# Kernel tuning notes

Hardware: AMD Instinct MI355X
Metric: run time of the kernel (lower is better)

Reference implementation:

```python
import jax, jax.numpy as jnp
import numpy as np
from jax.scipy.special import erf

N = 8_388_608  # number of options in the book
R = 0.02       # risk-free rate (init arg r)
Q = 0.01       # dividend yield (init arg q)


def setup_inputs() -> dict:
    key = jax.random.key(0)
    k1, k2, k3, k4 = jax.random.split(key, 4)
    S0 = jax.random.uniform(k1, (N,), jnp.float32, 80.0, 120.0)
    K = jax.random.uniform(k2, (N,), jnp.float32, 80.0, 120.0)
    T = jax.random.uniform(k3, (N,), jnp.float32, 0.01, 2.0)
    vt = jax.random.uniform(k4, (N,), jnp.float32, 0.01, 0.2)
    return {"S0": S0, "K": K, "T": T, "vt": vt}


def reference(S0, K, T, vt):
    # Black-Scholes 'all' pricing: [n,4] = (call, put, digital_call, digital_put)
    inv_sqrt2 = 0.7071067811865476
    sv = jnp.sqrt(vt * T)
    d1 = (jnp.log(S0 / K) + (R - Q + vt * 0.5) * T) / sv
    d2 = d1 - sv
    N1 = 0.5 * (1.0 + erf(d1 * inv_sqrt2))
    N2 = 0.5 * (1.0 + erf(d2 * inv_sqrt2))
    disc_r = jnp.exp(-R * T)
    disc_q = jnp.exp(-Q * T)
    call = S0 * disc_q * N1 - K * disc_r * N2
    put = -S0 * disc_q * (1.0 - N1) + K * disc_r * (1.0 - N2)
    dig_call = disc_r * N2
    dig_put = disc_r * (1.0 - N2)
    # expired (T == 0) branch: intrinsic values / indicator payoffs
    expired = T == 0
    call = jnp.where(expired, jnp.maximum(S0 - K, 0.0), call)
    put = jnp.where(expired, jnp.maximum(K - S0, 0.0), put)
    dig_call = jnp.where(expired, (S0 > K).astype(S0.dtype), dig_call)
    dig_put = jnp.where(expired, (S0 <= K).astype(S0.dtype), dig_put)
    return jnp.stack([call, put, dig_call, dig_put], axis=-1)
```

## Files before the change

kernel.cpp:

```cpp
#include <hip/hip_runtime.h>
#include <hip/hip_bf16.h>


#define BS_R 0.02f
#define BS_Q 0.01f

__device__ __forceinline__ void bs_one(float s, float k, float t, float v,
                                       float4& o) {
    const float inv_sqrt2 = 0.7071067811865476f;
    float sv = sqrtf(v * t);
    float d1 = (logf(s / k) + (BS_R - BS_Q + v * 0.5f) * t) / sv;
    float d2 = d1 - sv;
    float N1 = 0.5f * (1.0f + erff(d1 * inv_sqrt2));
    float N2 = 0.5f * (1.0f + erff(d2 * inv_sqrt2));
    float disc_r = expf(-BS_R * t);
    float disc_q = expf(-BS_Q * t);
    float call = s * disc_q * N1 - k * disc_r * N2;
    float put  = -s * disc_q * (1.0f - N1) + k * disc_r * (1.0f - N2);
    float dc = disc_r * N2;
    float dp = disc_r * (1.0f - N2);
    bool expired = (t == 0.0f);
    if (expired) {
        call = fmaxf(s - k, 0.0f);
        put  = fmaxf(k - s, 0.0f);
        dc   = (s > k) ? 1.0f : 0.0f;
        dp   = (s <= k) ? 1.0f : 0.0f;
    }
    o.x = call; o.y = put; o.z = dc; o.w = dp;
}

__global__ void __launch_bounds__(256)
bs_all_kernel(const float4* __restrict__ S0, const float4* __restrict__ K,
              const float4* __restrict__ T, const float4* __restrict__ vt,
              float4* __restrict__ out, int n4) {
    int stride = gridDim.x * blockDim.x;
    for (int i = blockIdx.x * blockDim.x + threadIdx.x; i < n4; i += stride) {
        float4 s = S0[i];
        float4 k = K[i];
        float4 t = T[i];
        float4 v = vt[i];
        float4 o0, o1, o2, o3;
        bs_one(s.x, k.x, t.x, v.x, o0);
        bs_one(s.y, k.y, t.y, v.y, o1);
        bs_one(s.z, k.z, t.z, v.z, o2);
        bs_one(s.w, k.w, t.w, v.w, o3);
        float4* op = out + (size_t)i * 4;
        op[0] = o0; op[1] = o1; op[2] = o2; op[3] = o3;
    }
}

extern "C" void kernel_launch(void* const* d_in, const int* in_sizes, int n_in,
                              void* d_out, int out_size, void* d_ws, size_t ws_size,
                              hipStream_t stream) {
    const float* S0 = (const float*)d_in[0];
    const float* K  = (const float*)d_in[1];
    const float* T  = (const float*)d_in[2];
    const float* vt = (const float*)d_in[3];
    float* out = (float*)d_out;
    int n = in_sizes[0];
    int n4 = n / 4;

    int block = 256;
    int grid = (n4 + block - 1) / block;
    if (grid > 2048) grid = 2048;
    bs_all_kernel<<<grid, block, 0, stream>>>(
        (const float4*)S0, (const float4*)K, (const float4*)T, (const float4*)vt,
        (float4*)out, n4);
}
```

Before: 251.6 us.

## Replace erf with logistic CDF approximation and use fast hardware intrinsics

Computes the normal CDF with a logistic approximation built from exp2 and rcp intrinsics instead of erff. It also uses native log2, exp2 and rsq builtins, derives the put and digital put via parity, and processes one option per thread with coalesced scalar loads. The aim is to remove the heavy transcendental arithmetic cost. In exchange it adds approximation error in the CDF and in the fast intrinsics.

```diff
diff --git a/kernel.cpp b/kernel.cpp
--- a/kernel.cpp
+++ b/kernel.cpp
@@ -2,50 +2,53 @@
 #include <hip/hip_bf16.h>
 
 
-#define BS_R 0.02f
-#define BS_Q 0.01f
+__global__ void __launch_bounds__(256)
+bs_all_kernel(const float* __restrict__ S0, const float* __restrict__ K,
+              const float* __restrict__ T, const float* __restrict__ vt,
+              float4* __restrict__ out, int n) {
+    const float LN2 = 0.69314718055994531f;
+    const float A   = -2.3048706f;
+    const float B   = -0.10180522f;
+    const float CR  = -0.028853901f;
+    const float CQ  = -0.014426951f;
 
-__device__ __forceinline__ void bs_one(float s, float k, float t, float v,
-                                       float4& o) {
-    const float inv_sqrt2 = 0.7071067811865476f;
-    float sv = sqrtf(v * t);
-    float d1 = (logf(s / k) + (BS_R - BS_Q + v * 0.5f) * t) / sv;
-    float d2 = d1 - sv;
-    float N1 = 0.5f * (1.0f + erff(d1 * inv_sqrt2));
-    float N2 = 0.5f * (1.0f + erff(d2 * inv_sqrt2));
-    float disc_r = expf(-BS_R * t);
-    float disc_q = expf(-BS_Q * t);
-    float call = s * disc_q * N1 - k * disc_r * N2;
-    float put  = -s * disc_q * (1.0f - N1) + k * disc_r * (1.0f - N2);
-    float dc = disc_r * N2;
-    float dp = disc_r * (1.0f - N2);
-    bool expired = (t == 0.0f);
-    if (expired) {
-        call = fmaxf(s - k, 0.0f);
-        put  = fmaxf(k - s, 0.0f);
-        dc   = (s > k) ? 1.0f : 0.0f;
-        dp   = (s <= k) ? 1.0f : 0.0f;
-    }
-    o.x = call; o.y = put; o.z = dc; o.w = dp;
-}
+    int stride = gridDim.x * blockDim.x;
+    for (int i = blockIdx.x * blockDim.x + threadIdx.x; i < n; i += stride) {
+        float s = S0[i];
+        float k = K[i];
+        float t = T[i];
+        float v = vt[i];
 
-__global__ void __launch_bounds__(256)
-bs_all_kernel(const float4* __restrict__ S0, const float4* __restrict__ K,
-              const float4* __restrict__ T, const float4* __restrict__ vt,
-              float4* __restrict__ out, int n4) {
-    int stride = gridDim.x * blockDim.x;
-    for (int i = blockIdx.x * blockDim.x + threadIdx.x; i < n4; i += stride) {
-        float4 s = S0[i];
-        float4 k = K[i];
-        float4 t = T[i];
-        float4 v = vt[i];
-        float4 o0, o1, o2, o3;
-        bs_one(s.x, k.x, t.x, v.x, o0);
-        bs_one(s.y, k.y, t.y, v.y, o1);
-        bs_one(s.z, k.z, t.z, v.z, o2);
-        bs_one(s.w, k.w, t.w, v.w, o3);
-        float4* op = out + (size_t)i * 4;
-        op[0] = o0; op[1] = o1; op[2] = o2; op[3] = o3;
+        float x      = v * t;
+        float inv_sv = __builtin_amdgcn_rsqf(x);
+        float sv     = x * inv_sv;
+
+        float lg = (__builtin_amdgcn_logf(s) - __builtin_amdgcn_logf(k)) * LN2;
+        float d1 = (lg + fmaf(0.5f, v, 0.01f) * t) * inv_sv;
+        float d2 = d1 - sv;
+
+        float a1 = d1 * fmaf(B, d1 * d1, A);
+        float a2 = d2 * fmaf(B, d2 * d2, A);
+        float N1 = __builtin_amdgcn_rcpf(1.0f + __builtin_amdgcn_exp2f(a1));
+        float N2 = __builtin_amdgcn_rcpf(1.0f + __builtin_amdgcn_exp2f(a2));
+
+        float disc_r = __builtin_amdgcn_exp2f(CR * t);
+        float disc_q = __builtin_amdgcn_exp2f(CQ * t);
+
+        float sq = s * disc_q;
+        float kr = k * disc_r;
+        float call = fmaf(sq, N1, -kr * N2);
+        float put  = call - sq + kr;
+        float dc   = disc_r * N2;
+        float dp   = disc_r - dc;
+
+        bool e = (t == 0.0f);
+        call = e ? fmaxf(s - k, 0.0f) : call;
+        put  = e ? fmaxf(k - s, 0.0f) : put;
+        dc   = e ? ((s > k)  ? 1.0f : 0.0f) : dc;
+        dp   = e ? ((s <= k) ? 1.0f : 0.0f) : dp;
+
+        out[i] = make_float4(call, put, dc, dp);
     }
 }
 
@@ -58,12 +61,8 @@
     const float* vt = (const float*)d_in[3];
     float* out = (float*)d_out;
     int n = in_sizes[0];
-    int n4 = n / 4;
 
     int block = 256;
-    int grid = (n4 + block - 1) / block;
-    if (grid > 2048) grid = 2048;
-    bs_all_kernel<<<grid, block, 0, stream>>>(
-        (const float4*)S0, (const float4*)K, (const float4*)T, (const float4*)vt,
-        (float4*)out, n4);
+    int grid = 2048;
+    bs_all_kernel<<<grid, block, 0, stream>>>(S0, K, T, vt, (float4*)out, n);
 }
```

New measurement: 242.9 us. 1.04x faster.
